# Kernel tuning notes

Hardware: AMD Instinct MI355X
Metric: run time of the kernel (lower is better)

Reference implementation:

```python
import jax, jax.numpy as jnp
import numpy as np

N = 8192       # num nodes
F_IN = 256     # num_features
NHID = 128     # nhid
E = 524288     # num edges (avg degree 64)
K = 32         # num_edge_preseve


def setup_inputs() -> dict:
    key = jax.random.key(0)
    ks = jax.random.split(key, 5)
    x = jax.random.normal(ks[0], (N, F_IN), jnp.float32)
    edge_index = jax.random.randint(ks[1], (2, E), 0, N, jnp.int32)
    W1 = jax.random.normal(ks[2], (F_IN, NHID), jnp.float32) / np.sqrt(F_IN)
    b1 = jnp.zeros((NHID,), jnp.float32)
    We = jax.random.normal(ks[3], (2 * NHID, 1), jnp.float32) / np.sqrt(2 * NHID)
    be = jnp.zeros((1,), jnp.float32)
    return {"x": x, "edge_index": edge_index, "W1": W1, "b1": b1, "We": We, "be": be}


def _segment_sparsemax(z, seg, num_segments):
    """Sparsemax applied independently within each segment (row) of an edge list."""
    E_ = z.shape[0]
    # group edges by segment, descending score within segment
    order = jnp.lexsort((-z, seg))
    zs = z[order]
    ss = seg[order]
    counts = jnp.zeros((num_segments,), jnp.int32).at[seg].add(1)
    starts = jnp.cumsum(counts) - counts                 # first sorted index of each segment
    pos = jnp.arange(E_, dtype=jnp.int32) - starts[ss]   # 0-based rank within segment
    cs = jnp.cumsum(zs)
    prefix = cs - zs                                     # cumsum excluding self
    seg_cs = cs - prefix[starts][ss]                     # within-segment inclusive cumsum
    j1 = (pos + 1).astype(zs.dtype)
    cond = 1.0 + j1 * zs > seg_cs                        # sparsemax support condition
    kmax = jax.ops.segment_max(jnp.where(cond, pos + 1, 0), ss, num_segments=num_segments)
    kmax = jnp.maximum(kmax, 1)                          # nonempty segments always have k>=1
    idx = jnp.clip(starts + kmax - 1, 0, E_ - 1)
    seg_cs_at_k = cs[idx] - prefix[jnp.clip(starts, 0, E_ - 1)]
    tau = (seg_cs_at_k - 1.0) / kmax.astype(zs.dtype)
    out_sorted = jnp.maximum(zs - tau[ss], 0.0)
    return jnp.zeros_like(z).at[order].set(out_sorted)


def reference(x, edge_index, W1, b1, We, be):
    h = jax.nn.relu(x @ W1 + b1)                 # [N, NHID]
    row, col = edge_index[0], edge_index[1]
    # edge score: Linear on concat([h[row], h[col]]) == split matmul (avoids [E, 2*NHID] concat)
    e = h[row] @ We[:NHID, 0] + h[col] @ We[NHID:, 0] + be[0]   # [E]
    scores = _segment_sparsemax(e, row, N)       # row-segmented sparsemax
    adj = jnp.zeros((N, N), h.dtype).at[row, col].set(scores)
    topv = jax.lax.top_k(adj, K)[0]              # [N, K], sorted descending
    thresh = topv[:, -1:]                        # per-row k-th largest value
    new_adj = jnp.where(adj >= thresh, adj, jnp.zeros((), adj.dtype))
    # original returns dense_to_sparse(new_adj) (data-dependent shape);
    # we return the equivalent masked dense adjacency.
    return h, new_adj
```

## Files before the change

### kernel.cpp

```cpp
#include <hip/hip_runtime.h>

#define N_    8192
#define FIN_  256
#define NHID_ 128
#define E_    524288
#define KTOP  32
#define CAP   160

__global__ __launch_bounds__(256) void k_fused(const float* __restrict__ x,
                                               const int* __restrict__ ei,
                                               const float* __restrict__ W1,
                                               const float* __restrict__ b1,
                                               const float* __restrict__ We,
                                               float* __restrict__ h,
                                               float* __restrict__ a,
                                               float* __restrict__ b,
                                               int* __restrict__ cnt,
                                               int* __restrict__ ecol) {
    __shared__ float xs[16][FIN_];
    int t = threadIdx.x;
    int blk = blockIdx.x;

    {
        int4 r4 = ((const int4*)ei)[blk * 256 + t];
        int4 c4 = ((const int4*)(ei + E_))[blk * 256 + t];
        int p;
        p = atomicAdd(&cnt[r4.x], 1); if (p < CAP) ecol[r4.x * CAP + p] = c4.x;
        p = atomicAdd(&cnt[r4.y], 1); if (p < CAP) ecol[r4.y * CAP + p] = c4.y;
        p = atomicAdd(&cnt[r4.z], 1); if (p < CAP) ecol[r4.z * CAP + p] = c4.z;
        p = atomicAdd(&cnt[r4.w], 1); if (p < CAP) ecol[r4.w * CAP + p] = c4.w;
    }

    int row0 = blk * 16;
    const float4* xg = (const float4*)(x + (size_t)row0 * FIN_);
    float4* xs4 = (float4*)&xs[0][0];
#pragma unroll
    for (int i = 0; i < 4; ++i) xs4[t + 256 * i] = xg[t + 256 * i];
    __syncthreads();

    int rg = t >> 5;
    int jg = t & 31;
    int r0 = 2 * rg, r1 = 2 * rg + 1;
    const float* wp = W1 + jg * 4;
    float4 bb = *(const float4*)(b1 + jg * 4);
    float4 acc0 = bb, acc1 = bb;
    const float* xr0 = xs[r0];
    const float* xr1 = xs[r1];
#pragma unroll 8
    for (int k = 0; k < FIN_; ++k) {
        float4 w = *(const float4*)(wp + (size_t)k * NHID_);
        float x0 = xr0[k], x1 = xr1[k];
        acc0.x = fmaf(x0, w.x, acc0.x);
        acc0.y = fmaf(x0, w.y, acc0.y);
        acc0.z = fmaf(x0, w.z, acc0.z);
        acc0.w = fmaf(x0, w.w, acc0.w);
        acc1.x = fmaf(x1, w.x, acc1.x);
        acc1.y = fmaf(x1, w.y, acc1.y);
        acc1.z = fmaf(x1, w.z, acc1.z);
        acc1.w = fmaf(x1, w.w, acc1.w);
    }
    acc0.x = fmaxf(acc0.x, 0.f); acc0.y = fmaxf(acc0.y, 0.f);
    acc0.z = fmaxf(acc0.z, 0.f); acc0.w = fmaxf(acc0.w, 0.f);
    acc1.x = fmaxf(acc1.x, 0.f); acc1.y = fmaxf(acc1.y, 0.f);
    acc1.z = fmaxf(acc1.z, 0.f); acc1.w = fmaxf(acc1.w, 0.f);
    *(float4*)(h + (size_t)(row0 + r0) * NHID_ + jg * 4) = acc0;
    *(float4*)(h + (size_t)(row0 + r1) * NHID_ + jg * 4) = acc1;

    float4 we1 = *(const float4*)(We + jg * 4);
    float4 we2 = *(const float4*)(We + NHID_ + jg * 4);
    float p0 = acc0.x * we1.x + acc0.y * we1.y + acc0.z * we1.z + acc0.w * we1.w;
    float q0 = acc0.x * we2.x + acc0.y * we2.y + acc0.z * we2.z + acc0.w * we2.w;
    float p1 = acc1.x * we1.x + acc1.y * we1.y + acc1.z * we1.z + acc1.w * we1.w;
    float q1 = acc1.x * we2.x + acc1.y * we2.y + acc1.z * we2.z + acc1.w * we2.w;
#pragma unroll
    for (int o = 16; o > 0; o >>= 1) {
        p0 += __shfl_down(p0, o, 32);
        q0 += __shfl_down(q0, o, 32);
        p1 += __shfl_down(p1, o, 32);
        q1 += __shfl_down(q1, o, 32);
    }
    if (jg == 0) {
        a[row0 + r0] = p0; b[row0 + r0] = q0;
        a[row0 + r1] = p1; b[row0 + r1] = q1;
    }
}

__global__ __launch_bounds__(256) void k_rows(const int* __restrict__ cnt,
                                              const int* __restrict__ ecol,
                                              const float* __restrict__ a,
                                              const float* __restrict__ b,
                                              const float* __restrict__ be,
                                              float* __restrict__ adj) {
    __shared__ float zs[CAP];
    __shared__ int   cols[CAP];
    __shared__ float srt[CAP];
    __shared__ unsigned char dupf[CAP];
    __shared__ float s_tau, s_thresh;

    int r = blockIdx.x;
    int t = threadIdx.x;
    int m = cnt[r];
    if (m > CAP) m = CAP;

    float* row = adj + (size_t)r * N_;
    float4* row4 = (float4*)row;
    float4 z4 = make_float4(0.f, 0.f, 0.f, 0.f);
#pragma unroll
    for (int i = 0; i < 8; ++i) row4[t + 256 * i] = z4;

    float ab = a[r] + be[0];
    for (int i = t; i < m; i += 256) {
        int c = ecol[r * CAP + i];
        cols[i] = c;
        zs[i] = ab + b[c];
    }
    __syncthreads();
    if (m == 0) return;

    for (int i = t; i < m; i += 256) {
        float zi = zs[i];
        int ci = cols[i];
        int rank = 0;
        for (int jj = 0; jj < m; ++jj) {
            float zj = zs[jj];
            rank += (zj > zi) || (zj == zi && jj < i);
        }
        bool dup = false;
        for (int jj = 0; jj < i; ++jj)
            if (cols[jj] == ci) { dup = true; break; }
        srt[rank] = zi;
        dupf[i] = dup ? 1 : 0;
    }
    __syncthreads();

    if (t == 0) {
        float c = 0.f;
        int kmax = 1;
        float csk = srt[0];
        for (int jj = 0; jj < m; ++jj) {
            c += srt[jj];
            if (1.0f + (float)(jj + 1) * srt[jj] > c) { kmax = jj + 1; csk = c; }
        }
        s_tau = (csk - 1.0f) / (float)kmax;
        s_thresh = 0.f;
    }
    __syncthreads();
    float tau = s_tau;

    for (int i = t; i < m; i += 256) {
        if (dupf[i]) continue;
        float zi = zs[i];
        int rank = 0;
        for (int jj = 0; jj < m; ++jj) {
            if (dupf[jj] || jj == i) continue;
            float zj = zs[jj];
            rank += (zj > zi) || (zj == zi && jj < i);
        }
        if (rank == KTOP - 1) {
            float s = zi - tau;
            s_thresh = s > 0.f ? s : 0.f;
        }
    }
    __syncthreads();
    float thresh = s_thresh;

    for (int i = t; i < m; i += 256) {
        float s = zs[i] - tau;
        if (s > 0.f && s >= thresh) row[cols[i]] = s;
    }
}

extern "C" void kernel_launch(void* const* d_in, const int* in_sizes, int n_in,
                              void* d_out, int out_size, void* d_ws, size_t ws_size,
                              hipStream_t stream) {
    const float* x  = (const float*)d_in[0];
    const int*   ei = (const int*)d_in[1];
    const float* W1 = (const float*)d_in[2];
    const float* b1 = (const float*)d_in[3];
    const float* We = (const float*)d_in[4];
    const float* be = (const float*)d_in[5];

    float* h_out   = (float*)d_out;
    float* adj_out = h_out + (size_t)N_ * NHID_;

    float* a    = (float*)d_ws;
    float* b    = a + N_;
    int*   cnt  = (int*)(b + N_);
    int*   ecol = cnt + N_;

    hipMemsetAsync(cnt, 0, N_ * sizeof(int), stream);
    k_fused<<<512, 256, 0, stream>>>(x, ei, W1, b1, We, h_out, a, b, cnt, ecol);
    k_rows <<<N_, 256, 0, stream>>>(cnt, ecol, a, b, be, adj_out);
}
```

Baseline: 375.5 us.

## Write each adjacency row once via shared bitmap and hash, store columns as ushort

Instead of zero-filling each 32KB adjacency row and then scattering the kept scores into global memory, each block now records the kept columns in a shared-memory bitmap plus an open-addressing hash of values. It then writes the row in a single coalesced float4 pass that fills in the nonzeros. The edge column buffer is also narrowed to 16-bit indices to halve its traffic. The cost is extra shared memory and hash probing, and duplicate edges are now skipped explicitly in the scatter.

```diff
diff --git a/kernel.cpp b/kernel.cpp
--- a/kernel.cpp
+++ b/kernel.cpp
@@ -6,6 +6,9 @@
 #define E_    524288
 #define KTOP  32
 #define CAP   160
+#define HASHSZ 512
+
+typedef unsigned short ushort_t;
 
 __global__ __launch_bounds__(256) void k_fused(const float* __restrict__ x,
                                                const int* __restrict__ ei,
@@ -16,7 +19,7 @@
                                                float* __restrict__ a,
                                                float* __restrict__ b,
                                                int* __restrict__ cnt,
-                                               int* __restrict__ ecol) {
+                                               ushort_t* __restrict__ ecol) {
     __shared__ float xs[16][FIN_];
     int t = threadIdx.x;
     int blk = blockIdx.x;
@@ -25,10 +28,10 @@
         int4 r4 = ((const int4*)ei)[blk * 256 + t];
         int4 c4 = ((const int4*)(ei + E_))[blk * 256 + t];
         int p;
-        p = atomicAdd(&cnt[r4.x], 1); if (p < CAP) ecol[r4.x * CAP + p] = c4.x;
-        p = atomicAdd(&cnt[r4.y], 1); if (p < CAP) ecol[r4.y * CAP + p] = c4.y;
-        p = atomicAdd(&cnt[r4.z], 1); if (p < CAP) ecol[r4.z * CAP + p] = c4.z;
-        p = atomicAdd(&cnt[r4.w], 1); if (p < CAP) ecol[r4.w * CAP + p] = c4.w;
+        p = atomicAdd(&cnt[r4.x], 1); if (p < CAP) ecol[r4.x * CAP + p] = (ushort_t)c4.x;
+        p = atomicAdd(&cnt[r4.y], 1); if (p < CAP) ecol[r4.y * CAP + p] = (ushort_t)c4.y;
+        p = atomicAdd(&cnt[r4.z], 1); if (p < CAP) ecol[r4.z * CAP + p] = (ushort_t)c4.z;
+        p = atomicAdd(&cnt[r4.w], 1); if (p < CAP) ecol[r4.w * CAP + p] = (ushort_t)c4.w;
     }
 
     int row0 = blk * 16;
@@ -86,7 +89,7 @@
 }
 
 __global__ __launch_bounds__(256) void k_rows(const int* __restrict__ cnt,
-                                              const int* __restrict__ ecol,
+                                              const ushort_t* __restrict__ ecol,
                                               const float* __restrict__ a,
                                               const float* __restrict__ b,
                                               const float* __restrict__ be,
@@ -95,6 +98,9 @@
     __shared__ int   cols[CAP];
     __shared__ float srt[CAP];
     __shared__ unsigned char dupf[CAP];
+    __shared__ unsigned int bitmap[N_ / 32];
+    __shared__ int   hcol[HASHSZ];
+    __shared__ float hval[HASHSZ];
     __shared__ float s_tau, s_thresh;
 
     int r = blockIdx.x;
@@ -102,71 +108,105 @@
     int m = cnt[r];
     if (m > CAP) m = CAP;
 
-    float* row = adj + (size_t)r * N_;
-    float4* row4 = (float4*)row;
-    float4 z4 = make_float4(0.f, 0.f, 0.f, 0.f);
-#pragma unroll
-    for (int i = 0; i < 8; ++i) row4[t + 256 * i] = z4;
+    bitmap[t] = 0u;
+    hcol[t] = -1;
+    hcol[t + 256] = -1;
 
     float ab = a[r] + be[0];
     for (int i = t; i < m; i += 256) {
-        int c = ecol[r * CAP + i];
+        int c = (int)ecol[r * CAP + i];
         cols[i] = c;
         zs[i] = ab + b[c];
     }
     __syncthreads();
-    if (m == 0) return;
-
-    for (int i = t; i < m; i += 256) {
-        float zi = zs[i];
-        int ci = cols[i];
-        int rank = 0;
-        for (int jj = 0; jj < m; ++jj) {
-            float zj = zs[jj];
-            rank += (zj > zi) || (zj == zi && jj < i);
-        }
-        bool dup = false;
-        for (int jj = 0; jj < i; ++jj)
-            if (cols[jj] == ci) { dup = true; break; }
-        srt[rank] = zi;
-        dupf[i] = dup ? 1 : 0;
+
+    if (m > 0) {
+        for (int i = t; i < m; i += 256) {
+            float zi = zs[i];
+            int ci = cols[i];
+            int rank = 0;
+            for (int jj = 0; jj < m; ++jj) {
+                float zj = zs[jj];
+                rank += (zj > zi) || (zj == zi && jj < i);
+            }
+            bool dup = false;
+            for (int jj = 0; jj < i; ++jj)
+                if (cols[jj] == ci) { dup = true; break; }
+            srt[rank] = zi;
+            dupf[i] = dup ? 1 : 0;
+        }
+        __syncthreads();
+
+        if (t == 0) {
+            float c = 0.f;
+            int kmax = 1;
+            float csk = srt[0];
+            for (int jj = 0; jj < m; ++jj) {
+                c += srt[jj];
+                if (1.0f + (float)(jj + 1) * srt[jj] > c) { kmax = jj + 1; csk = c; }
+            }
+            s_tau = (csk - 1.0f) / (float)kmax;
+            s_thresh = 0.f;
+        }
+        __syncthreads();
+        float tau = s_tau;
+
+        for (int i = t; i < m; i += 256) {
+            if (dupf[i]) continue;
+            float zi = zs[i];
+            int rank = 0;
+            for (int jj = 0; jj < m; ++jj) {
+                if (dupf[jj] || jj == i) continue;
+                float zj = zs[jj];
+                rank += (zj > zi) || (zj == zi && jj < i);
+            }
+            if (rank == KTOP - 1) {
+                float s = zi - tau;
+                s_thresh = s > 0.f ? s : 0.f;
+            }
+        }
+        __syncthreads();
+        float thresh = s_thresh;
+
+        for (int i = t; i < m; i += 256) {
+            if (dupf[i]) continue;
+            float s = zs[i] - tau;
+            if (s > 0.f && s >= thresh) {
+                int c = cols[i];
+                atomicOr(&bitmap[c >> 5], 1u << (c & 31));
+                int slot = c & (HASHSZ - 1);
+                while (atomicCAS(&hcol[slot], -1, c) != -1)
+                    slot = (slot + 1) & (HASHSZ - 1);
+                hval[slot] = s;
+            }
+        }
     }
     __syncthreads();
 
-    if (t == 0) {
-        float c = 0.f;
-        int kmax = 1;
-        float csk = srt[0];
-        for (int jj = 0; jj < m; ++jj) {
-            c += srt[jj];
-            if (1.0f + (float)(jj + 1) * srt[jj] > c) { kmax = jj + 1; csk = c; }
-        }
-        s_tau = (csk - 1.0f) / (float)kmax;
-        s_thresh = 0.f;
-    }
-    __syncthreads();
-    float tau = s_tau;
-
-    for (int i = t; i < m; i += 256) {
-        if (dupf[i]) continue;
-        float zi = zs[i];
-        int rank = 0;
-        for (int jj = 0; jj < m; ++jj) {
-            if (dupf[jj] || jj == i) continue;
-            float zj = zs[jj];
-            rank += (zj > zi) || (zj == zi && jj < i);
-        }
-        if (rank == KTOP - 1) {
-            float s = zi - tau;
-            s_thresh = s > 0.f ? s : 0.f;
-        }
-    }
-    __syncthreads();
-    float thresh = s_thresh;
-
-    for (int i = t; i < m; i += 256) {
-        float s = zs[i] - tau;
-        if (s > 0.f && s >= thresh) row[cols[i]] = s;
+    float4* row4 = (float4*)(adj + (size_t)r * N_);
+#pragma unroll
+    for (int k2 = 0; k2 < 8; ++k2) {
+        int idx = t + 256 * k2;
+        unsigned int word = bitmap[idx >> 3];
+        unsigned int nib = (word >> ((idx & 7) * 4)) & 0xFu;
+        float4 v = make_float4(0.f, 0.f, 0.f, 0.f);
+        if (nib) {
+            int cbase = idx * 4;
+#pragma unroll
+            for (int bbit = 0; bbit < 4; ++bbit) {
+                if (nib & (1u << bbit)) {
+                    int c = cbase + bbit;
+                    int slot = c & (HASHSZ - 1);
+                    while (hcol[slot] != c) slot = (slot + 1) & (HASHSZ - 1);
+                    float val = hval[slot];
+                    if (bbit == 0) v.x = val;
+                    else if (bbit == 1) v.y = val;
+                    else if (bbit == 2) v.z = val;
+                    else v.w = val;
+                }
+            }
+        }
+        row4[idx] = v;
     }
 }
 
@@ -183,10 +223,10 @@
     float* h_out   = (float*)d_out;
     float* adj_out = h_out + (size_t)N_ * NHID_;
 
-    float* a    = (float*)d_ws;
-    float* b    = a + N_;
-    int*   cnt  = (int*)(b + N_);
-    int*   ecol = cnt + N_;
+    float*    a    = (float*)d_ws;
+    float*    b    = a + N_;
+    int*      cnt  = (int*)(b + N_);
+    ushort_t* ecol = (ushort_t*)(cnt + N_);
 
     hipMemsetAsync(cnt, 0, N_ * sizeof(int), stream);
     k_fused<<<512, 256, 0, stream>>>(x, ei, W1, b1, We, h_out, a, b, cnt, ecol);
```

Measured after the change: 371.1 us. No clear change (-1.2%).
